# Optimization experiments

Hardware: AMD Instinct MI355X
Metric: run time of the kernel (lower is better)

Reference implementation:

```python
import jax, jax.numpy as jnp
import numpy as np

N, F, H = 100000, 128, 2
DH = F // H  # per-head dim = 64
E = 1600000


def setup_inputs() -> dict:
    key = jax.random.key(0)
    ks = jax.random.split(key, 10)
    s = 0.05
    return {
        "nodes": jax.random.normal(ks[0], (N, F), jnp.float32),
        "edge_index": jax.random.randint(ks[1], (2, E), 0, N, jnp.int64),
        # TransformerConv linear layers (stored as [in, out] so we do x @ W)
        "Wq": jax.random.normal(ks[2], (F, F), jnp.float32) * s,
        "bq": jnp.zeros((F,), jnp.float32),
        "Wk": jax.random.normal(ks[3], (F, F), jnp.float32) * s,
        "bk": jnp.zeros((F,), jnp.float32),
        "Wv": jax.random.normal(ks[4], (F, F), jnp.float32) * s,
        "bv": jnp.zeros((F,), jnp.float32),
        "Wskip": jax.random.normal(ks[5], (F, F), jnp.float32) * s,
        "bskip": jnp.zeros((F,), jnp.float32),
        # gate: Linear(2F, F, bias=False); fuse: Linear(F, F, bias=False)
        "Wgate": jax.random.normal(ks[6], (2 * F, F), jnp.float32) * s,
        "Wfuse": jax.random.normal(ks[7], (F, F), jnp.float32) * s,
    }


def transformer_conv(nodes, src, dst, Wq, bq, Wk, bk, Wv, bv, Wskip, bskip):
    n = nodes.shape[0]
    q = (nodes @ Wq + bq).reshape(n, H, DH)
    k = (nodes @ Wk + bk).reshape(n, H, DH)
    v = (nodes @ Wv + bv).reshape(n, H, DH)
    # per-edge attention logits: [E, H]
    alpha = jnp.einsum("ehd,ehd->eh", q[dst], k[src]) / jnp.sqrt(jnp.float32(DH))
    # segment softmax over incoming edges of each destination node
    amax = jax.ops.segment_max(alpha, dst, num_segments=n)  # [N, H]
    ex = jnp.exp(alpha - amax[dst])
    denom = jax.ops.segment_sum(ex, dst, num_segments=n)  # [N, H]
    w = ex / denom[dst]  # [E, H]
    msg = v[src] * w[:, :, None]  # [E, H, DH]
    agg = jax.ops.segment_sum(msg, dst, num_segments=n).reshape(n, F)
    # root/skip connection (beta=0 -> plain add)
    return agg + nodes @ Wskip + bskip


def reference(nodes, edge_index, Wq, bq, Wk, bk, Wv, bv, Wskip, bskip, Wgate, Wfuse):
    src, dst = edge_index[0], edge_index[1]
    x = transformer_conv(nodes, src, dst, Wq, bq, Wk, bk, Wv, bv, Wskip, bskip)
    h = jnp.concatenate([nodes, x], axis=-1)  # [N, 2F]
    gate = jax.nn.sigmoid(h @ Wgate)  # [N, F]
    fuse = jnp.tanh(x @ Wfuse)  # [N, F]
    return gate * fuse + (1.0 - gate) * nodes
```

## Files before the change

kernel.cpp:

```cpp
#include <hip/hip_runtime.h>
#include <hip/hip_fp8.h>
#include <stdint.h>

#define NN 100000
#define EE 1600000
#define FF 128
#define CAP 60

typedef __attribute__((ext_vector_type(8)))  short bf16x8;
typedef __attribute__((ext_vector_type(8)))  unsigned short u16x8;
typedef __attribute__((ext_vector_type(2)))  float f32x2;
typedef __attribute__((ext_vector_type(16))) float f32x16;

#define NB_BLOCKS    6250
#define PREP_BLOCKS  450
#define CNT0_BLOCKS  98
#define BUILD2_BLOCKS 1563
#define QKVS_BLOCKS  12500
#define F2_BLOCKS    (BUILD2_BLOCKS + QKVS_BLOCKS)

#define QSCALE 0.1803368801111244f

__device__ __forceinline__ float bf2f(unsigned short u) {
    union { unsigned int i; float f; } c; c.i = ((unsigned int)u) << 16; return c.f;
}
__device__ __forceinline__ unsigned short f2bf(float f) {
    union { unsigned int i; float f; } c; c.f = f;
    unsigned int u = c.i;
    return (unsigned short)((u + 0x7FFFu + ((u >> 16) & 1u)) >> 16);
}
__device__ __forceinline__ float fp82f(unsigned int b) {
    __hip_fp8_e4m3 t; t.__x = (__hip_fp8_storage_t)(b & 0xFFu); return (float)t;
}
__device__ __forceinline__ unsigned char f2fp8(float f) {
    __hip_fp8_e4m3 t(f); return (unsigned char)t.__x;
}
template<bool HI>
__device__ __forceinline__ f32x2 cvtpk8(unsigned int w) {
#if __has_builtin(__builtin_amdgcn_cvt_pk_f32_fp8)
    return __builtin_amdgcn_cvt_pk_f32_fp8((int)w, HI);
#else
    f32x2 r;
    r[0] = fp82f(HI ? (w >> 16) : w);
    r[1] = fp82f(HI ? (w >> 24) : (w >> 8));
    return r;
#endif
}
__device__ __forceinline__ bf16x8 pack8(const float* p) {
    float4 f0 = *(const float4*)p;
    float4 f1 = *(const float4*)(p + 4);
    bf16x8 r;
    r[0] = (short)f2bf(f0.x); r[1] = (short)f2bf(f0.y);
    r[2] = (short)f2bf(f0.z); r[3] = (short)f2bf(f0.w);
    r[4] = (short)f2bf(f1.x); r[5] = (short)f2bf(f1.y);
    r[6] = (short)f2bf(f1.z); r[7] = (short)f2bf(f1.w);
    return r;
}

__global__ __launch_bounds__(256) void k_f1(
    const float* __restrict__ nodes, unsigned short* __restrict__ nb,
    const float* __restrict__ Wq, const float* __restrict__ Wk,
    const float* __restrict__ Wv, const float* __restrict__ Ws,
    const float* __restrict__ Wg, const float* __restrict__ Wf,
    const float* __restrict__ bq, const float* __restrict__ bk,
    const float* __restrict__ bv, const float* __restrict__ bs,
    unsigned short* __restrict__ Wp, unsigned short* __restrict__ Wp2,
    float* __restrict__ bias, int* __restrict__ count)
{
    const int bid = blockIdx.x;
    if (bid < NB_BLOCKS) {
        size_t i = ((size_t)bid * 256 + threadIdx.x) * 8;
        *(bf16x8*)(nb + i) = pack8(nodes + i);
    } else if (bid < NB_BLOCKS + PREP_BLOCKS) {
        int idx = (bid - NB_BLOCKS) * 256 + threadIdx.x;
        if (idx < 65536) {
            int j = idx & 7, lane = (idx >> 3) & 63, ks = (idx >> 9) & 7;
            int cf = (idx >> 12) & 3, cg = idx >> 14;
            int c  = cf * 32 + (lane & 31);
            int kk = ks * 16 + (lane >> 5) * 8 + j;
            const float* W = (cg == 0) ? Wq : (cg == 1) ? Wk : (cg == 2) ? Wv : Ws;
            Wp[idx] = f2bf(W[kk * FF + c]);
        } else if (idx < 65536 + 49152) {
            int p = idx - 65536;
            int j = p & 7, lane = (p >> 3) & 63, ks = (p >> 9) & 7;
            int cf = (p >> 12) & 3, mat = p >> 14;
            int c  = cf * 32 + (lane & 31);
            int kk = ks * 16 + (lane >> 5) * 8 + j;
            float v = (mat == 0) ? Wg[kk * FF + c]
                    : (mat == 1) ? Wg[(FF + kk) * FF + c]
                                 : Wf[kk * FF + c];
            Wp2[p] = f2bf(v);
        } else if (idx < 65536 + 49152 + 512) {
            int j = idx - (65536 + 49152);
            float b = (j < 128) ? bq[j] : (j < 256) ? bk[j - 128]
                    : (j < 384) ? bv[j - 256] : bs[j - 384];
            bias[j] = b;
        }
    } else {
        int j = ((bid - NB_BLOCKS - PREP_BLOCKS) * 256 + threadIdx.x) * 4;
        if (j < NN) *(int4*)(count + j) = make_int4(0, 0, 0, 0);
    }
}

__global__ __launch_bounds__(256) void k_f2(
    const int* __restrict__ src, const int* __restrict__ dst,
    int* __restrict__ count, int* __restrict__ srclist,
    const unsigned short* __restrict__ nb, const unsigned short* __restrict__ Wp,
    const float* __restrict__ bias, unsigned short* __restrict__ qb,
    unsigned char* __restrict__ kvb, unsigned short* __restrict__ skb)
{
    const int bid = blockIdx.x;
    if (bid % 9 == 0) {
        const int bb = bid / 9;
        const int e0 = bb * 1024 + threadIdx.x;
        #pragma unroll
        for (int j = 0; j < 4; ++j) {
            const int e = e0 + j * 256;
            if (e < EE) {
                int d = dst[e];
                int s = src[e];
                int r = atomicAdd(&count[d], 1);
                if (r < CAP) __builtin_nontemporal_store(s, &srclist[(size_t)d * CAP + r]);
            }
        }
        return;
    }
    const int q = bid - bid / 9 - 1;
    const int row0 = (q >> 2) * 32;
    const int cg = q & 3;
    const int wave = threadIdx.x >> 6, lane = threadIdx.x & 63;
    const int arow = row0 + (lane & 31);
    const int khalf = lane >> 5;
    const int cf = wave;

    f32x16 acc;
    #pragma unroll
    for (int r = 0; r < 16; ++r) acc[r] = 0.f;

    const unsigned short* ap = nb + (size_t)arow * FF + khalf * 8;
    #pragma unroll
    for (int ks = 0; ks < 8; ++ks) {
        bf16x8 a = *(const bf16x8*)(ap + ks * 16);
        bf16x8 b = *(const bf16x8*)(Wp + (((cg * 4 + cf) * 8 + ks) << 9) + (lane << 3));
        acc = __builtin_amdgcn_mfma_f32_32x32x16_bf16(a, b, acc, 0, 0, 0);
    }

    const int col = cf * 32 + (lane & 31);
    const float bv = bias[cg * 128 + col];
    #pragma unroll
    for (int r = 0; r < 16; ++r) {
        const int rr = row0 + (r & 3) + 8 * (r >> 2) + 4 * (lane >> 5);
        const float fv = acc[r] + bv;
        if (cg == 0)      qb [(size_t)rr * 128 + col] = f2bf(fv);
        else if (cg == 1) kvb[(size_t)rr * 256 + (col >> 2) * 8 + (col & 3)]     = f2fp8(fv);
        else if (cg == 2) kvb[(size_t)rr * 256 + (col >> 2) * 8 + 4 + (col & 3)] = f2fp8(fv);
        else              skb[(size_t)rr * 128 + col] = f2bf(fv);
    }
}

__global__ __launch_bounds__(256, 4) void k_f3(
    const unsigned short* __restrict__ nb, const unsigned short* __restrict__ qb,
    const unsigned char* __restrict__ kvb, const unsigned short* __restrict__ skb,
    const unsigned short* __restrict__ Wp2,
    const int* __restrict__ count, const int* __restrict__ srclist,
    float* __restrict__ out)
{
    __shared__ unsigned short xl[32 * 128];
    const int wave = threadIdx.x >> 6, lane = threadIdx.x & 63;
    const int row0 = blockIdx.x * 32;

    const int es = lane >> 4;
    const int le = lane & 15;
    const int slane = lane < CAP ? lane : CAP - 1;

    int   deg_n  = count[row0 + wave * 8];
    u16x8 qr_n   = *(const u16x8*)(qb  + (size_t)(row0 + wave * 8) * FF + le * 8);
    int   sreg_n = srclist[(size_t)(row0 + wave * 8) * CAP + slane];
    u16x8 sr_n   = *(const u16x8*)(skb + (size_t)(row0 + wave * 8) * FF + le * 8);

    #pragma unroll 1
    for (int i = 0; i < 8; ++i) {
        const int rl  = wave * 8 + i;
        const int wid = row0 + rl;

        int deg = __builtin_amdgcn_readfirstlane(deg_n);
        if (deg > CAP) deg = CAP;
        const u16x8 qr  = qr_n;
        const int   sreg = sreg_n;
        const u16x8 sr  = sr_n;

        if (i < 7) {
            const int widn = wid + 1;
            deg_n  = count[widn];
            qr_n   = *(const u16x8*)(qb  + (size_t)widn * FF + le * 8);
            sreg_n = srclist[(size_t)widn * CAP + slane];
            sr_n   = *(const u16x8*)(skb + (size_t)widn * FF + le * 8);
        }

        f32x2 qa0, qa1, qa2, qa3;
        qa0[0] = bf2f(qr[0]) * QSCALE; qa0[1] = bf2f(qr[1]) * QSCALE;
        qa1[0] = bf2f(qr[2]) * QSCALE; qa1[1] = bf2f(qr[3]) * QSCALE;
        qa2[0] = bf2f(qr[4]) * QSCALE; qa2[1] = bf2f(qr[5]) * QSCALE;
        qa3[0] = bf2f(qr[6]) * QSCALE; qa3[1] = bf2f(qr[7]) * QSCALE;

        float denom = 0.f;
        f32x2 a01 = {0.f, 0.f}, a23 = {0.f, 0.f}, a45 = {0.f, 0.f}, a67 = {0.f, 0.f};

        const int nit = (deg + 3) >> 2;
        #pragma unroll 4
        for (int it = 0; it < nit; ++it) {
            const int idx  = 4 * it + es;
            const int sidx = idx < deg ? idx : deg - 1;
            const int s    = __shfl(sreg, sidx);
            const uint4 kv = *(const uint4*)(kvb + (size_t)s * 256 + le * 16);
            f32x2 pp = qa0 * cvtpk8<false>(kv.x);
            pp += qa1 * cvtpk8<true>(kv.x);
            pp += qa2 * cvtpk8<false>(kv.z);
            pp += qa3 * cvtpk8<true>(kv.z);
            float p = pp[0] + pp[1];
            p += __shfl_xor(p, 1);
            p += __shfl_xor(p, 2);
            p += __shfl_xor(p, 4);
            const float ex = (idx < deg) ? exp2f(p) : 0.f;
            denom += ex;
            f32x2 exv; exv[0] = ex; exv[1] = ex;
            a01 += exv * cvtpk8<false>(kv.y);
            a23 += exv * cvtpk8<true>(kv.y);
            a45 += exv * cvtpk8<false>(kv.w);
            a67 += exv * cvtpk8<true>(kv.w);
        }
        denom += __shfl_xor(denom, 16);
        denom += __shfl_xor(denom, 32);
        float af[8] = {a01[0], a01[1], a23[0], a23[1], a45[0], a45[1], a67[0], a67[1]};
        #pragma unroll
        for (int j = 0; j < 8; ++j) {
            af[j] += __shfl_xor(af[j], 16);
            af[j] += __shfl_xor(af[j], 32);
        }

        if (es == 0) {
            const float inv = (denom > 0.f) ? (1.0f / denom) : 0.f;
            u16x8 o;
            #pragma unroll
            for (int j = 0; j < 8; ++j) o[j] = f2bf(fmaf(af[j], inv, bf2f(sr[j])));
            *(u16x8*)&xl[rl * 128 + ((le ^ (rl & 7)) << 3)] = o;
        }
    }
    __syncthreads();

    const int arow = row0 + (lane & 31);
    const int khalf = lane >> 5;
    const int cf = wave;

    f32x16 gacc, facc;
    #pragma unroll
    for (int r = 0; r < 16; ++r) { gacc[r] = 0.f; facc[r] = 0.f; }

    #pragma unroll
    for (int ks = 0; ks < 8; ++ks) {
        bf16x8 an = *(const bf16x8*)(nb + (size_t)arow * FF + ks * 16 + khalf * 8);
        const int g2 = ks * 2 + khalf;
        bf16x8 ax = *(const bf16x8*)&xl[(lane & 31) * 128 + ((g2 ^ ((lane & 31) & 7)) << 3)];
        bf16x8 b0 = *(const bf16x8*)(Wp2 + (((0 * 4 + cf) * 8 + ks) << 9) + (lane << 3));
        bf16x8 b1 = *(const bf16x8*)(Wp2 + (((1 * 4 + cf) * 8 + ks) << 9) + (lane << 3));
        bf16x8 b2 = *(const bf16x8*)(Wp2 + (((2 * 4 + cf) * 8 + ks) << 9) + (lane << 3));
        gacc = __builtin_amdgcn_mfma_f32_32x32x16_bf16(an, b0, gacc, 0, 0, 0);
        gacc = __builtin_amdgcn_mfma_f32_32x32x16_bf16(ax, b1, gacc, 0, 0, 0);
        facc = __builtin_amdgcn_mfma_f32_32x32x16_bf16(ax, b2, facc, 0, 0, 0);
    }

    const int col = cf * 32 + (lane & 31);
    #pragma unroll
    for (int r = 0; r < 16; ++r) {
        const int rr = row0 + (r & 3) + 8 * (r >> 2) + 4 * (lane >> 5);
        const float g  = 1.0f / (1.0f + __expf(-gacc[r]));
        const float e2 = __expf(2.0f * facc[r]);
        const float fv = (e2 - 1.0f) / (e2 + 1.0f);
        const float nv = bf2f(nb[(size_t)rr * FF + col]);
        out[(size_t)rr * FF + col] = g * fv + (1.0f - g) * nv;
    }
}

extern "C" void kernel_launch(void* const* d_in, const int* in_sizes, int n_in,
                              void* d_out, int out_size, void* d_ws, size_t ws_size,
                              hipStream_t stream) {
    const float* nodes = (const float*)d_in[0];
    const int*   ei    = (const int*)d_in[1];
    const int*   esrc  = ei;
    const int*   edst  = ei + EE;
    const float* Wq = (const float*)d_in[2];
    const float* bq = (const float*)d_in[3];
    const float* Wk = (const float*)d_in[4];
    const float* bk = (const float*)d_in[5];
    const float* Wv = (const float*)d_in[6];
    const float* bv = (const float*)d_in[7];
    const float* Ws = (const float*)d_in[8];
    const float* bs = (const float*)d_in[9];
    const float* Wg = (const float*)d_in[10];
    const float* Wf = (const float*)d_in[11];
    float* out = (float*)d_out;

    char* wsb = (char*)d_ws;
    unsigned short* qb   = (unsigned short*)wsb;
    unsigned char*  kvb  = (unsigned char*)(qb + (size_t)NN * 128);
    unsigned short* skb  = (unsigned short*)(kvb + (size_t)NN * 256);
    unsigned short* nb   = skb + (size_t)NN * 128;
    unsigned short* Wp   = nb + (size_t)NN * 128;
    unsigned short* Wp2  = Wp + 65536;
    float* bias  = (float*)(Wp2 + 49152);
    int* count   = (int*)(bias + 512);
    int* srclist = count + NN;

    k_f1<<<NB_BLOCKS + PREP_BLOCKS + CNT0_BLOCKS, 256, 0, stream>>>(
        nodes, nb, Wq, Wk, Wv, Ws, Wg, Wf, bq, bk, bv, bs, Wp, Wp2, bias, count);
    k_f2<<<F2_BLOCKS, 256, 0, stream>>>(
        esrc, edst, count, srclist, nb, Wp, bias, qb, kvb, skb);
    k_f3<<<NN / 32, 256, 0, stream>>>(
        nb, qb, kvb, skb, Wp2, count, srclist, out);
}
```

Measured before the change: 219.5 us.

## Replicate per-node edge counters and drop bf16 node copy pass

```diff
diff --git a/kernel.cpp b/kernel.cpp
--- a/kernel.cpp
+++ b/kernel.cpp
@@ -5,19 +5,19 @@
 #define NN 100000
 #define EE 1600000
 #define FF 128
-#define CAP 60
+#define NREP 8
+#define RCAP 16
 
 typedef __attribute__((ext_vector_type(8)))  short bf16x8;
 typedef __attribute__((ext_vector_type(8)))  unsigned short u16x8;
 typedef __attribute__((ext_vector_type(2)))  float f32x2;
 typedef __attribute__((ext_vector_type(16))) float f32x16;
 
-#define NB_BLOCKS    6250
 #define PREP_BLOCKS  450
-#define CNT0_BLOCKS  98
-#define BUILD2_BLOCKS 1563
+#define CNT0_BLOCKS  782
+#define F1_BLOCKS    (PREP_BLOCKS + CNT0_BLOCKS)
 #define QKVS_BLOCKS  12500
-#define F2_BLOCKS    (BUILD2_BLOCKS + QKVS_BLOCKS)
+#define F2_BLOCKS    14063
 
 #define QSCALE 0.1803368801111244f
 
@@ -58,21 +58,17 @@
 }
 
 __global__ __launch_bounds__(256) void k_f1(
-    const float* __restrict__ nodes, unsigned short* __restrict__ nb,
     const float* __restrict__ Wq, const float* __restrict__ Wk,
     const float* __restrict__ Wv, const float* __restrict__ Ws,
     const float* __restrict__ Wg, const float* __restrict__ Wf,
     const float* __restrict__ bq, const float* __restrict__ bk,
     const float* __restrict__ bv, const float* __restrict__ bs,
     unsigned short* __restrict__ Wp, unsigned short* __restrict__ Wp2,
-    float* __restrict__ bias, int* __restrict__ count)
+    float* __restrict__ bias, int* __restrict__ count8)
 {
     const int bid = blockIdx.x;
-    if (bid < NB_BLOCKS) {
-        size_t i = ((size_t)bid * 256 + threadIdx.x) * 8;
-        *(bf16x8*)(nb + i) = pack8(nodes + i);
-    } else if (bid < NB_BLOCKS + PREP_BLOCKS) {
-        int idx = (bid - NB_BLOCKS) * 256 + threadIdx.x;
+    if (bid < PREP_BLOCKS) {
+        int idx = bid * 256 + threadIdx.x;
         if (idx < 65536) {
             int j = idx & 7, lane = (idx >> 3) & 63, ks = (idx >> 9) & 7;
             int cf = (idx >> 12) & 3, cg = idx >> 14;
@@ -97,21 +93,22 @@
             bias[j] = b;
         }
     } else {
-        int j = ((bid - NB_BLOCKS - PREP_BLOCKS) * 256 + threadIdx.x) * 4;
-        if (j < NN) *(int4*)(count + j) = make_int4(0, 0, 0, 0);
+        int j = ((bid - PREP_BLOCKS) * 256 + threadIdx.x) * 4;
+        if (j < NREP * NN) *(int4*)(count8 + j) = make_int4(0, 0, 0, 0);
     }
 }
 
 __global__ __launch_bounds__(256) void k_f2(
     const int* __restrict__ src, const int* __restrict__ dst,
-    int* __restrict__ count, int* __restrict__ srclist,
-    const unsigned short* __restrict__ nb, const unsigned short* __restrict__ Wp,
+    int* __restrict__ count8, int* __restrict__ srclist,
+    const float* __restrict__ nodes, const unsigned short* __restrict__ Wp,
     const float* __restrict__ bias, unsigned short* __restrict__ qb,
     unsigned char* __restrict__ kvb, unsigned short* __restrict__ skb)
 {
     const int bid = blockIdx.x;
     if (bid % 9 == 0) {
         const int bb = bid / 9;
+        const int rep = bid & 7;
         const int e0 = bb * 1024 + threadIdx.x;
         #pragma unroll
         for (int j = 0; j < 4; ++j) {
@@ -119,8 +116,8 @@
             if (e < EE) {
                 int d = dst[e];
                 int s = src[e];
-                int r = atomicAdd(&count[d], 1);
-                if (r < CAP) __builtin_nontemporal_store(s, &srclist[(size_t)d * CAP + r]);
+                int r = atomicAdd(&count8[(size_t)rep * NN + d], 1);
+                if (r < RCAP) srclist[(size_t)d * 128 + rep * RCAP + r] = s;
             }
         }
         return;
@@ -137,10 +134,10 @@
     #pragma unroll
     for (int r = 0; r < 16; ++r) acc[r] = 0.f;
 
-    const unsigned short* ap = nb + (size_t)arow * FF + khalf * 8;
+    const float* ap = nodes + (size_t)arow * FF + khalf * 8;
     #pragma unroll
     for (int ks = 0; ks < 8; ++ks) {
-        bf16x8 a = *(const bf16x8*)(ap + ks * 16);
+        bf16x8 a = pack8(ap + ks * 16);
         bf16x8 b = *(const bf16x8*)(Wp + (((cg * 4 + cf) * 8 + ks) << 9) + (lane << 3));
         acc = __builtin_amdgcn_mfma_f32_32x32x16_bf16(a, b, acc, 0, 0, 0);
     }
@@ -159,10 +156,10 @@
 }
 
 __global__ __launch_bounds__(256, 4) void k_f3(
-    const unsigned short* __restrict__ nb, const unsigned short* __restrict__ qb,
+    const float* __restrict__ nodes, const unsigned short* __restrict__ qb,
     const unsigned char* __restrict__ kvb, const unsigned short* __restrict__ skb,
     const unsigned short* __restrict__ Wp2,
-    const int* __restrict__ count, const int* __restrict__ srclist,
+    const int* __restrict__ count8, const int* __restrict__ srclist,
     float* __restrict__ out)
 {
     __shared__ unsigned short xl[32 * 128];
@@ -171,30 +168,44 @@
 
     const int es = lane >> 4;
     const int le = lane & 15;
-    const int slane = lane < CAP ? lane : CAP - 1;
-
-    int   deg_n  = count[row0 + wave * 8];
-    u16x8 qr_n   = *(const u16x8*)(qb  + (size_t)(row0 + wave * 8) * FF + le * 8);
-    int   sreg_n = srclist[(size_t)(row0 + wave * 8) * CAP + slane];
-    u16x8 sr_n   = *(const u16x8*)(skb + (size_t)(row0 + wave * 8) * FF + le * 8);
+
+    int cn[8];
+    {
+        const int w0 = row0 + wave * 8;
+        #pragma unroll
+        for (int p = 0; p < 8; ++p) cn[p] = count8[(size_t)p * NN + w0];
+    }
+    u16x8 qr_n = *(const u16x8*)(qb  + (size_t)(row0 + wave * 8) * FF + le * 8);
+    u16x8 sr_n = *(const u16x8*)(skb + (size_t)(row0 + wave * 8) * FF + le * 8);
 
     #pragma unroll 1
     for (int i = 0; i < 8; ++i) {
         const int rl  = wave * 8 + i;
         const int wid = row0 + rl;
 
-        int deg = __builtin_amdgcn_readfirstlane(deg_n);
-        if (deg > CAP) deg = CAP;
-        const u16x8 qr  = qr_n;
-        const int   sreg = sreg_n;
-        const u16x8 sr  = sr_n;
+        int c[8], deg = 0;
+        #pragma unroll
+        for (int p = 0; p < 8; ++p) { c[p] = cn[p] > RCAP ? RCAP : cn[p]; deg += c[p]; }
+        if (deg > 64) deg = 64;
+        const u16x8 qr = qr_n;
+        const u16x8 sr = sr_n;
+
+        const int li = (deg > 0) ? (lane < deg ? lane : deg - 1) : 0;
+        int rep = 0, off = 0, base = 0;
+        #pragma unroll
+        for (int p = 0; p < 8; ++p) {
+            const bool in = (li >= base) && (li < base + c[p]);
+            if (in) { rep = p; off = li - base; }
+            base += c[p];
+        }
+        const int sreg = srclist[(size_t)wid * 128 + rep * RCAP + off];
 
         if (i < 7) {
             const int widn = wid + 1;
-            deg_n  = count[widn];
-            qr_n   = *(const u16x8*)(qb  + (size_t)widn * FF + le * 8);
-            sreg_n = srclist[(size_t)widn * CAP + slane];
-            sr_n   = *(const u16x8*)(skb + (size_t)widn * FF + le * 8);
+            #pragma unroll
+            for (int p = 0; p < 8; ++p) cn[p] = count8[(size_t)p * NN + widn];
+            qr_n = *(const u16x8*)(qb  + (size_t)widn * FF + le * 8);
+            sr_n = *(const u16x8*)(skb + (size_t)widn * FF + le * 8);
         }
 
         f32x2 qa0, qa1, qa2, qa3;
@@ -258,7 +269,7 @@
 
     #pragma unroll
     for (int ks = 0; ks < 8; ++ks) {
-        bf16x8 an = *(const bf16x8*)(nb + (size_t)arow * FF + ks * 16 + khalf * 8);
+        bf16x8 an = pack8(nodes + (size_t)arow * FF + ks * 16 + khalf * 8);
         const int g2 = ks * 2 + khalf;
         bf16x8 ax = *(const bf16x8*)&xl[(lane & 31) * 128 + ((g2 ^ ((lane & 31) & 7)) << 3)];
         bf16x8 b0 = *(const bf16x8*)(Wp2 + (((0 * 4 + cf) * 8 + ks) << 9) + (lane << 3));
@@ -276,7 +287,7 @@
         const float g  = 1.0f / (1.0f + __expf(-gacc[r]));
         const float e2 = __expf(2.0f * facc[r]);
         const float fv = (e2 - 1.0f) / (e2 + 1.0f);
-        const float nv = bf2f(nb[(size_t)rr * FF + col]);
+        const float nv = nodes[(size_t)rr * FF + col];
         out[(size_t)rr * FF + col] = g * fv + (1.0f - g) * nv;
     }
 }
@@ -304,17 +315,16 @@
     unsigned short* qb   = (unsigned short*)wsb;
     unsigned char*  kvb  = (unsigned char*)(qb + (size_t)NN * 128);
     unsigned short* skb  = (unsigned short*)(kvb + (size_t)NN * 256);
-    unsigned short* nb   = skb + (size_t)NN * 128;
-    unsigned short* Wp   = nb + (size_t)NN * 128;
+    unsigned short* Wp   = skb + (size_t)NN * 128;
     unsigned short* Wp2  = Wp + 65536;
-    float* bias  = (float*)(Wp2 + 49152);
-    int* count   = (int*)(bias + 512);
-    int* srclist = count + NN;
-
-    k_f1<<<NB_BLOCKS + PREP_BLOCKS + CNT0_BLOCKS, 256, 0, stream>>>(
-        nodes, nb, Wq, Wk, Wv, Ws, Wg, Wf, bq, bk, bv, bs, Wp, Wp2, bias, count);
+    float* bias   = (float*)(Wp2 + 49152);
+    int* count8   = (int*)(bias + 512);
+    int* srclist  = count8 + (size_t)NREP * NN;
+
+    k_f1<<<F1_BLOCKS, 256, 0, stream>>>(
+        Wq, Wk, Wv, Ws, Wg, Wf, bq, bk, bv, bs, Wp, Wp2, bias, count8);
     k_f2<<<F2_BLOCKS, 256, 0, stream>>>(
-        esrc, edst, count, srclist, nb, Wp, bias, qb, kvb, skb);
+        esrc, edst, count8, srclist, nodes, Wp, bias, qb, kvb, skb);
     k_f3<<<NN / 32, 256, 0, stream>>>(
-        nb, qb, kvb, skb, Wp2, count, srclist, out);
-}
+        nodes, qb, kvb, skb, Wp2, count8, srclist, out);
+}
```

New measurement: 260.5 us. 1.19x slower.

## Drop bf16 node copy; convert fp32 nodes inline in GEMM kernels

Applied to the files above, without the earlier changes.

```diff
diff --git a/kernel.cpp b/kernel.cpp
--- a/kernel.cpp
+++ b/kernel.cpp
@@ -12,12 +12,12 @@
 typedef __attribute__((ext_vector_type(2)))  float f32x2;
 typedef __attribute__((ext_vector_type(16))) float f32x16;
 
-#define NB_BLOCKS    6250
 #define PREP_BLOCKS  450
 #define CNT0_BLOCKS  98
-#define BUILD2_BLOCKS 1563
+#define F1_BLOCKS    (PREP_BLOCKS + CNT0_BLOCKS)
+#define BUILD_BLOCKS 782
 #define QKVS_BLOCKS  12500
-#define F2_BLOCKS    (BUILD2_BLOCKS + QKVS_BLOCKS)
+#define F2_BLOCKS    (QKVS_BLOCKS + BUILD_BLOCKS)
 
 #define QSCALE 0.1803368801111244f
 
@@ -58,7 +58,6 @@
 }
 
 __global__ __launch_bounds__(256) void k_f1(
-    const float* __restrict__ nodes, unsigned short* __restrict__ nb,
     const float* __restrict__ Wq, const float* __restrict__ Wk,
     const float* __restrict__ Wv, const float* __restrict__ Ws,
     const float* __restrict__ Wg, const float* __restrict__ Wf,
@@ -68,11 +67,8 @@
     float* __restrict__ bias, int* __restrict__ count)
 {
     const int bid = blockIdx.x;
-    if (bid < NB_BLOCKS) {
-        size_t i = ((size_t)bid * 256 + threadIdx.x) * 8;
-        *(bf16x8*)(nb + i) = pack8(nodes + i);
-    } else if (bid < NB_BLOCKS + PREP_BLOCKS) {
-        int idx = (bid - NB_BLOCKS) * 256 + threadIdx.x;
+    if (bid < PREP_BLOCKS) {
+        int idx = bid * 256 + threadIdx.x;
         if (idx < 65536) {
             int j = idx & 7, lane = (idx >> 3) & 63, ks = (idx >> 9) & 7;
             int cf = (idx >> 12) & 3, cg = idx >> 14;
@@ -97,7 +93,7 @@
             bias[j] = b;
         }
     } else {
-        int j = ((bid - NB_BLOCKS - PREP_BLOCKS) * 256 + threadIdx.x) * 4;
+        int j = ((bid - PREP_BLOCKS) * 256 + threadIdx.x) * 4;
         if (j < NN) *(int4*)(count + j) = make_int4(0, 0, 0, 0);
     }
 }
@@ -105,16 +101,16 @@
 __global__ __launch_bounds__(256) void k_f2(
     const int* __restrict__ src, const int* __restrict__ dst,
     int* __restrict__ count, int* __restrict__ srclist,
-    const unsigned short* __restrict__ nb, const unsigned short* __restrict__ Wp,
+    const float* __restrict__ nodes, const unsigned short* __restrict__ Wp,
     const float* __restrict__ bias, unsigned short* __restrict__ qb,
     unsigned char* __restrict__ kvb, unsigned short* __restrict__ skb)
 {
     const int bid = blockIdx.x;
-    if (bid % 9 == 0) {
-        const int bb = bid / 9;
-        const int e0 = bb * 1024 + threadIdx.x;
+    if (bid % 17 == 0) {
+        const int bb = bid / 17;
+        const int e0 = bb * 2048 + threadIdx.x;
         #pragma unroll
-        for (int j = 0; j < 4; ++j) {
+        for (int j = 0; j < 8; ++j) {
             const int e = e0 + j * 256;
             if (e < EE) {
                 int d = dst[e];
@@ -125,7 +121,8 @@
         }
         return;
     }
-    const int q = bid - bid / 9 - 1;
+    const int nbb = bid / 17 + 1;
+    const int q = bid - (nbb < BUILD_BLOCKS ? nbb : BUILD_BLOCKS);
     const int row0 = (q >> 2) * 32;
     const int cg = q & 3;
     const int wave = threadIdx.x >> 6, lane = threadIdx.x & 63;
@@ -137,10 +134,10 @@
     #pragma unroll
     for (int r = 0; r < 16; ++r) acc[r] = 0.f;
 
-    const unsigned short* ap = nb + (size_t)arow * FF + khalf * 8;
+    const float* ap = nodes + (size_t)arow * FF + khalf * 8;
     #pragma unroll
     for (int ks = 0; ks < 8; ++ks) {
-        bf16x8 a = *(const bf16x8*)(ap + ks * 16);
+        bf16x8 a = pack8(ap + ks * 16);
         bf16x8 b = *(const bf16x8*)(Wp + (((cg * 4 + cf) * 8 + ks) << 9) + (lane << 3));
         acc = __builtin_amdgcn_mfma_f32_32x32x16_bf16(a, b, acc, 0, 0, 0);
     }
@@ -159,7 +156,7 @@
 }
 
 __global__ __launch_bounds__(256, 4) void k_f3(
-    const unsigned short* __restrict__ nb, const unsigned short* __restrict__ qb,
+    const float* __restrict__ nodes, const unsigned short* __restrict__ qb,
     const unsigned char* __restrict__ kvb, const unsigned short* __restrict__ skb,
     const unsigned short* __restrict__ Wp2,
     const int* __restrict__ count, const int* __restrict__ srclist,
@@ -258,7 +255,7 @@
 
     #pragma unroll
     for (int ks = 0; ks < 8; ++ks) {
-        bf16x8 an = *(const bf16x8*)(nb + (size_t)arow * FF + ks * 16 + khalf * 8);
+        bf16x8 an = pack8(nodes + (size_t)arow * FF + ks * 16 + khalf * 8);
         const int g2 = ks * 2 + khalf;
         bf16x8 ax = *(const bf16x8*)&xl[(lane & 31) * 128 + ((g2 ^ ((lane & 31) & 7)) << 3)];
         bf16x8 b0 = *(const bf16x8*)(Wp2 + (((0 * 4 + cf) * 8 + ks) << 9) + (lane << 3));
@@ -276,7 +273,7 @@
         const float g  = 1.0f / (1.0f + __expf(-gacc[r]));
         const float e2 = __expf(2.0f * facc[r]);
         const float fv = (e2 - 1.0f) / (e2 + 1.0f);
-        const float nv = bf2f(nb[(size_t)rr * FF + col]);
+        const float nv = nodes[(size_t)rr * FF + col];
         out[(size_t)rr * FF + col] = g * fv + (1.0f - g) * nv;
     }
 }
@@ -304,17 +301,16 @@
     unsigned short* qb   = (unsigned short*)wsb;
     unsigned char*  kvb  = (unsigned char*)(qb + (size_t)NN * 128);
     unsigned short* skb  = (unsigned short*)(kvb + (size_t)NN * 256);
-    unsigned short* nb   = skb + (size_t)NN * 128;
-    unsigned short* Wp   = nb + (size_t)NN * 128;
+    unsigned short* Wp   = skb + (size_t)NN * 128;
     unsigned short* Wp2  = Wp + 65536;
     float* bias  = (float*)(Wp2 + 49152);
     int* count   = (int*)(bias + 512);
     int* srclist = count + NN;
 
-    k_f1<<<NB_BLOCKS + PREP_BLOCKS + CNT0_BLOCKS, 256, 0, stream>>>(
-        nodes, nb, Wq, Wk, Wv, Ws, Wg, Wf, bq, bk, bv, bs, Wp, Wp2, bias, count);
+    k_f1<<<F1_BLOCKS, 256, 0, stream>>>(
+        Wq, Wk, Wv, Ws, Wg, Wf, bq, bk, bv, bs, Wp, Wp2, bias, count);
     k_f2<<<F2_BLOCKS, 256, 0, stream>>>(
-        esrc, edst, count, srclist, nb, Wp, bias, qb, kvb, skb);
+        esrc, edst, count, srclist, nodes, Wp, bias, qb, kvb, skb);
     k_f3<<<NN / 32, 256, 0, stream>>>(
-        nb, qb, kvb, skb, Wp2, count, srclist, out);
-}
+        nodes, qb, kvb, skb, Wp2, count, srclist, out);
+}
```

Measured after the change: 256.8 us. +17.0%, slower.

## Build adjacency via atomic-exchange linked list then compact into per-node slots

Applied to the files above, without the earlier changes.

```diff
diff --git a/kernel.cpp b/kernel.cpp
--- a/kernel.cpp
+++ b/kernel.cpp
@@ -14,7 +14,7 @@
 
 #define NB_BLOCKS    6250
 #define PREP_BLOCKS  450
-#define CNT0_BLOCKS  98
+#define HEAD0_BLOCKS 98
 #define BUILD2_BLOCKS 1563
 #define QKVS_BLOCKS  12500
 #define F2_BLOCKS    (BUILD2_BLOCKS + QKVS_BLOCKS)
@@ -65,7 +65,7 @@
     const float* __restrict__ bq, const float* __restrict__ bk,
     const float* __restrict__ bv, const float* __restrict__ bs,
     unsigned short* __restrict__ Wp, unsigned short* __restrict__ Wp2,
-    float* __restrict__ bias, int* __restrict__ count)
+    float* __restrict__ bias, int* __restrict__ head)
 {
     const int bid = blockIdx.x;
     if (bid < NB_BLOCKS) {
@@ -98,13 +98,13 @@
         }
     } else {
         int j = ((bid - NB_BLOCKS - PREP_BLOCKS) * 256 + threadIdx.x) * 4;
-        if (j < NN) *(int4*)(count + j) = make_int4(0, 0, 0, 0);
+        if (j < NN) *(int4*)(head + j) = make_int4(-1, -1, -1, -1);
     }
 }
 
 __global__ __launch_bounds__(256) void k_f2(
     const int* __restrict__ src, const int* __restrict__ dst,
-    int* __restrict__ count, int* __restrict__ srclist,
+    int* __restrict__ head, uint2* __restrict__ list,
     const unsigned short* __restrict__ nb, const unsigned short* __restrict__ Wp,
     const float* __restrict__ bias, unsigned short* __restrict__ qb,
     unsigned char* __restrict__ kvb, unsigned short* __restrict__ skb)
@@ -119,8 +119,8 @@
             if (e < EE) {
                 int d = dst[e];
                 int s = src[e];
-                int r = atomicAdd(&count[d], 1);
-                if (r < CAP) __builtin_nontemporal_store(s, &srclist[(size_t)d * CAP + r]);
+                int old = atomicExch(&head[d], e);
+                list[e] = make_uint2((unsigned)old, (unsigned)s);
             }
         }
         return;
@@ -156,6 +156,23 @@
         else if (cg == 2) kvb[(size_t)rr * 256 + (col >> 2) * 8 + 4 + (col & 3)] = f2fp8(fv);
         else              skb[(size_t)rr * 128 + col] = f2bf(fv);
     }
+}
+
+__global__ __launch_bounds__(256) void k_f2b(
+    const uint2* __restrict__ list, const int* __restrict__ head,
+    int* __restrict__ count, int* __restrict__ srclist)
+{
+    const int d = blockIdx.x * 256 + threadIdx.x;
+    if (d >= NN) return;
+    int e = head[d];
+    int n = 0;
+    while (e >= 0 && n < CAP) {
+        const uint2 p = list[e];
+        srclist[(size_t)d * CAP + n] = (int)p.y;
+        e = (int)p.x;
+        ++n;
+    }
+    count[d] = n;
 }
 
 __global__ __launch_bounds__(256, 4) void k_f3(
@@ -310,11 +327,14 @@
     float* bias  = (float*)(Wp2 + 49152);
     int* count   = (int*)(bias + 512);
     int* srclist = count + NN;
-
-    k_f1<<<NB_BLOCKS + PREP_BLOCKS + CNT0_BLOCKS, 256, 0, stream>>>(
-        nodes, nb, Wq, Wk, Wv, Ws, Wg, Wf, bq, bk, bv, bs, Wp, Wp2, bias, count);
+    int* head    = srclist + (size_t)NN * CAP;
+    uint2* list  = (uint2*)(head + NN);
+
+    k_f1<<<NB_BLOCKS + PREP_BLOCKS + HEAD0_BLOCKS, 256, 0, stream>>>(
+        nodes, nb, Wq, Wk, Wv, Ws, Wg, Wf, bq, bk, bv, bs, Wp, Wp2, bias, head);
     k_f2<<<F2_BLOCKS, 256, 0, stream>>>(
-        esrc, edst, count, srclist, nb, Wp, bias, qb, kvb, skb);
+        esrc, edst, head, list, nb, Wp, bias, qb, kvb, skb);
+    k_f2b<<<(NN + 255) / 256, 256, 0, stream>>>(list, head, count, srclist);
     k_f3<<<NN / 32, 256, 0, stream>>>(
         nb, qb, kvb, skb, Wp2, count, srclist, out);
 }
```

After: 248.0 us. 1.13x slower.
